# Performance work log

Hardware: AMD Instinct MI355X
Metric: run time of the kernel (lower is better)

Reference implementation:

```python
import jax, jax.numpy as jnp
import numpy as np

B_, H_, W_, DM = 32, 64, 64, 256
D_INNER, D_STATE, NHEADS, HEADDIM = 512, 64, 8, 64
D_IN_PROJ = D_INNER + 2 * D_STATE + NHEADS  # 648


def setup_inputs() -> dict:
    key = jax.random.key(0)
    ks = jax.random.split(key, 4)
    x = jax.random.normal(ks[0], (B_, H_, W_, DM), dtype=jnp.float32)
    W_in = jax.random.normal(ks[1], (DM, D_IN_PROJ), dtype=jnp.float32) * 0.05
    dt_bias = jax.random.normal(ks[2], (NHEADS,), dtype=jnp.float32)
    A_log = jax.random.uniform(ks[3], (NHEADS,), dtype=jnp.float32)  # A in [1, e)
    D_param = jnp.ones((NHEADS,), dtype=jnp.float32)
    ln_gamma = jnp.ones((D_INNER,), dtype=jnp.float32)
    ln_beta = jnp.zeros((D_INNER,), dtype=jnp.float32)
    W_out = jax.random.normal(jax.random.fold_in(key, 7), (D_INNER, DM), dtype=jnp.float32) * 0.05
    return {"x": x, "W_in": W_in, "dt_bias": dt_bias, "A_log": A_log,
            "D_param": D_param, "ln_gamma": ln_gamma, "ln_beta": ln_beta, "W_out": W_out}


def reference(x, W_in, dt_bias, A_log, D_param, ln_gamma, ln_beta, W_out):
    B, H, W, Dm = x.shape
    L = H * W
    u = x.reshape(B, L, Dm)
    A = -jnp.exp(A_log)  # (nheads,), negative
    xbcdt = u @ W_in  # (B, L, 648)
    x_ssm = xbcdt[..., :D_INNER]                          # (B, L, d_inner)
    B_ssm = xbcdt[..., D_INNER:D_INNER + D_STATE]         # (B, L, d_state) ~ K
    C_ssm = xbcdt[..., D_INNER + D_STATE:D_INNER + 2 * D_STATE]  # (B, L, d_state) ~ Q
    dt = jax.nn.softplus(xbcdt[..., D_INNER + 2 * D_STATE:] + dt_bias)  # (B, L, nheads)
    V = x_ssm.reshape(B, L, NHEADS, HEADDIM)  # (B, L, h, p)
    # dA gating: dt * A per head (defaults: no exp/softmax/norm variants)
    dA = dt * A  # (B, L, h)
    V_scaled = V * dA[..., None]  # (B, L, h, p)
    # linear-attention dual: KV = K^T @ V_scaled, then Q @ KV
    KV = jnp.einsum('bls,blhp->bhsp', B_ssm, V_scaled)  # (B, h, d_state, p)
    y = jnp.einsum('bls,bhsp->blhp', C_ssm, KV)         # (B, L, h, p)
    # D skip (per-head)
    y = y + V * D_param[None, None, :, None]
    y = y.reshape(B, L, D_INNER)
    # LayerNorm
    mu = jnp.mean(y, axis=-1, keepdims=True)
    var = jnp.var(y, axis=-1, keepdims=True)
    y = (y - mu) / jnp.sqrt(var + 1e-5) * ln_gamma + ln_beta
    out = y @ W_out
    return out.reshape(B, H, W, Dm)
```

## Files before the change

kernel.cpp:

```cpp
#include <hip/hip_runtime.h>
#include <hip/hip_bf16.h>
#include <math.h>

constexpr int B_N   = 32;
constexpr int L_N   = 4096;
constexpr int DM    = 256;
constexpr int DIN   = 512;
constexpr int DS    = 64;
constexpr int NH    = 8;
constexpr int HD    = 64;
constexpr int M_N   = B_N * L_N;
constexpr int XBW   = 640;
constexpr int YST   = 536;
constexpr int AST   = 268;

typedef unsigned short u16;
typedef short s16x4 __attribute__((ext_vector_type(4)));
typedef short s16x8 __attribute__((ext_vector_type(8)));
typedef float f32x4 __attribute__((ext_vector_type(4)));
typedef unsigned short u16x8 __attribute__((ext_vector_type(8)));
typedef unsigned short u16x4 __attribute__((ext_vector_type(4)));

__device__ __forceinline__ float softplusf(float z) {
  return (z > 20.f) ? z : log1pf(expf(z));
}
__device__ __forceinline__ u16 f2bf(float f) {
  unsigned u = __float_as_uint(f);
  u += 0x7FFFu + ((u >> 16) & 1u);
  return (u16)(u >> 16);
}
__device__ __forceinline__ float bf2f(u16 u) {
  return __uint_as_float(((unsigned)u) << 16);
}
__device__ __forceinline__ s16x8 ld_frag2(const short* p) {
  s16x4 lo = *(const s16x4*)p;
  s16x4 hi = *(const s16x4*)(p + 4);
  s16x8 r;
  r[0]=lo[0]; r[1]=lo[1]; r[2]=lo[2]; r[3]=lo[3];
  r[4]=hi[0]; r[5]=hi[1]; r[6]=hi[2]; r[7]=hi[3];
  return r;
}

#define GLDS(gsrc, ldst)                                                       \
  __builtin_amdgcn_global_load_lds(                                            \
      (const __attribute__((address_space(1))) void*)(gsrc),                   \
      (__attribute__((address_space(3))) void*)(ldst), 16, 0, 0)

constexpr long CW1 = 768L * 256;
constexpr long CW2 = CW1 + 256L * 512;
__global__ __launch_bounds__(256) void k_cvt(
    const float* __restrict__ Wi, const float* __restrict__ Wo,
    u16* __restrict__ WinT, u16* __restrict__ WoT) {
  for (long i = (long)blockIdx.x * 256 + threadIdx.x; i < CW2;
       i += (long)gridDim.x * 256) {
    if (i < CW1) {
      int n = (int)(i >> 8); int k = (int)(i & 255);
      WinT[i] = (n < 648) ? f2bf(Wi[(size_t)k * 648 + n]) : (u16)0;
    } else {
      long t = i - CW1; int n = (int)(t >> 9); int k = (int)(t & 511);
      WoT[t] = f2bf(Wo[(size_t)k * 256 + n]);
    }
  }
}

__global__ __launch_bounds__(256) void k_inproj(
    const float* __restrict__ x, const u16* __restrict__ WinT,
    const float* __restrict__ dt_bias, const float* __restrict__ A_log,
    u16* __restrict__ xbcdt, float* __restrict__ dAv) {
  __shared__ __align__(16) short sA[128 * AST];
  __shared__ __align__(16) short sB[128 * 32];
  const int tid = threadIdx.x;
  const int wave = tid >> 6, lane = tid & 63;
  const int m0 = blockIdx.x * 128;
  const int wr = wave >> 1, wc = wave & 1;
  const int fr = lane & 15, fq = lane >> 4;

#pragma unroll
  for (int q = 0; q < 32; ++q) {
    int idx = tid + q * 256;
    int row = idx >> 6, c4 = idx & 63;
    float4 v = *(const float4*)(x + (size_t)(m0 + row) * DM + c4 * 4);
    u16x4 o = {f2bf(v.x), f2bf(v.y), f2bf(v.z), f2bf(v.w)};
    *(u16x4*)&sA[row * AST + c4 * 4] = o;
  }
  __syncthreads();

  int rowB[2], kcB[2], ldsOffB[2];
#pragma unroll
  for (int q = 0; q < 2; ++q) {
    int G = wave * 128 + q * 64 + lane;
    rowB[q] = G >> 2; kcB[q] = G & 3;
    ldsOffB[q] = G * 8;
  }

  for (int nt = 0; nt < 6; ++nt) {
    const int n0 = nt * 128;
    f32x4 acc[4][4] = {};
    for (int k0 = 0; k0 < DM; k0 += 32) {
      if (nt || k0) __syncthreads();
#pragma unroll
      for (int q = 0; q < 2; ++q)
        GLDS(WinT + (size_t)(n0 + rowB[q]) * DM + kcB[q] * 8 + k0, sB + ldsOffB[q]);
      __syncthreads();
      const int kb = fq * 8;
      s16x8 af[4], bf[4];
#pragma unroll
      for (int i = 0; i < 4; ++i)
        af[i] = ld_frag2(&sA[(wr * 64 + i * 16 + fr) * AST + k0 + kb]);
#pragma unroll
      for (int j = 0; j < 4; ++j)
        bf[j] = *(const s16x8*)&sB[(wc * 64 + j * 16 + fr) * 32 + kb];
#pragma unroll
      for (int i = 0; i < 4; ++i)
#pragma unroll
        for (int j = 0; j < 4; ++j)
          acc[i][j] = __builtin_amdgcn_mfma_f32_16x16x32_bf16(af[i], bf[j], acc[i][j], 0, 0, 0);
    }
    const int row_base = m0 + wr * 64 + fq * 4;
    if (n0 < 640) {
      const int col_base = n0 + wc * 64;
#pragma unroll
      for (int i = 0; i < 4; ++i)
#pragma unroll
        for (int r = 0; r < 4; ++r) {
          int row = row_base + i * 16 + r;
#pragma unroll
          for (int j = 0; j < 4; ++j)
            xbcdt[(size_t)row * XBW + col_base + j * 16 + fr] = f2bf(acc[i][j][r]);
        }
    } else if (wc == 0 && fr < 8) {
      const float nAe = -expf(A_log[fr]);
      const float db = dt_bias[fr];
#pragma unroll
      for (int i = 0; i < 4; ++i)
#pragma unroll
        for (int r = 0; r < 4; ++r) {
          int row = row_base + i * 16 + r;
          dAv[(size_t)row * NH + fr] = softplusf(acc[i][0][r] + db) * nAe;
        }
    }
  }
}

__global__ __launch_bounds__(256) void k_bt(
    const u16* __restrict__ xbcdt, u16* __restrict__ Bt) {
  __shared__ u16 sT[64][72];
  const int m0 = blockIdx.x * 64;
  const int b  = m0 >> 12;
  const int l0 = m0 & (L_N - 1);
  const int tid = threadIdx.x;
#pragma unroll
  for (int q = 0; q < 2; ++q) {
    int r = (tid >> 3) + q * 32, c8 = (tid & 7) * 8;
    u16x8 v = *(const u16x8*)&xbcdt[(size_t)(m0 + r) * XBW + DIN + c8];
#pragma unroll
    for (int jj = 0; jj < 8; ++jj) sT[r][c8 + jj] = v[jj];
  }
  __syncthreads();
#pragma unroll
  for (int q = 0; q < 2; ++q) {
    int s = (tid >> 3) + q * 32, lc8 = (tid & 7) * 8;
    u16x8 o;
#pragma unroll
    for (int jj = 0; jj < 8; ++jj) o[jj] = sT[lc8 + jj][s];
    *(u16x8*)&Bt[((size_t)(b * 64 + s)) * L_N + l0 + lc8] = o;
  }
}

__global__ __launch_bounds__(256) void k_kv(
    const u16* __restrict__ xbcdt, const u16* __restrict__ Bt,
    const float* __restrict__ dAv, float* __restrict__ KVp) {
  const int bh = blockIdx.y;
  const int b = bh >> 3, h = bh & 7;
  const int l0 = blockIdx.x * (L_N / 4);
  const int tid = threadIdx.x;
  const int wave = tid >> 6, lane = tid & 63;
  const int wr = wave >> 1, wc = wave & 1;
  const int fr = lane & 15, fq = lane >> 4;
  __shared__ short sBt[64 * 36];
  __shared__ short sVt[64 * 36];
  f32x4 acc[2][2] = {};
  const int ts = tid >> 2, tlc = tid & 3;
  const int tl = tid >> 3, tpg = tid & 7;

  for (int ks = 0; ks < L_N / 4; ks += 32) {
    u16x8 vb = *(const u16x8*)&Bt[((size_t)(b * 64 + ts)) * L_N + l0 + ks + tlc * 8];
    const int gl = b * L_N + l0 + ks + tl;
    u16x8 vv = *(const u16x8*)&xbcdt[(size_t)gl * XBW + h * HD + tpg * 8];
    const float da = dAv[(size_t)gl * NH + h];
    __syncthreads();
    *(s16x4*)&sBt[ts * 36 + tlc * 8]     = *(s16x4*)&vb;
    *(s16x4*)&sBt[ts * 36 + tlc * 8 + 4] = *((s16x4*)&vb + 1);
#pragma unroll
    for (int jj = 0; jj < 8; ++jj)
      sVt[(tpg * 8 + jj) * 36 + tl] = (short)f2bf(bf2f(vv[jj]) * da);
    __syncthreads();
    s16x8 af[2], bf[2];
#pragma unroll
    for (int i = 0; i < 2; ++i)
      af[i] = ld_frag2(&sBt[(wr * 32 + i * 16 + fr) * 36 + fq * 8]);
#pragma unroll
    for (int j = 0; j < 2; ++j)
      bf[j] = ld_frag2(&sVt[(wc * 32 + j * 16 + fr) * 36 + fq * 8]);
#pragma unroll
    for (int i = 0; i < 2; ++i)
#pragma unroll
      for (int j = 0; j < 2; ++j)
        acc[i][j] = __builtin_amdgcn_mfma_f32_16x16x32_bf16(af[i], bf[j], acc[i][j], 0, 0, 0);
  }
  float* dst = KVp + ((size_t)(blockIdx.x * 256 + bh)) * 4096;
#pragma unroll
  for (int i = 0; i < 2; ++i)
#pragma unroll
    for (int j = 0; j < 2; ++j) {
      int p = wc * 32 + j * 16 + fr;
      int s0 = wr * 32 + i * 16 + fq * 4;
      float4 v;
      v.x = acc[i][j][0]; v.y = acc[i][j][1];
      v.z = acc[i][j][2]; v.w = acc[i][j][3];
      *(float4*)&dst[p * 64 + s0] = v;
    }
}

__global__ __launch_bounds__(256) void k_kvsum(
    const float* __restrict__ KVp, u16* __restrict__ KVt) {
  const int bh = blockIdx.x;
  const int tid = threadIdx.x;
  const float* src = KVp + (size_t)bh * 4096;
#pragma unroll
  for (int q = 0; q < 4; ++q) {
    int i4 = (tid + q * 256) * 4;
    float4 v0 = *(const float4*)(src + i4);
    float4 v1 = *(const float4*)(src + 1048576 + i4);
    float4 v2 = *(const float4*)(src + 2097152 + i4);
    float4 v3 = *(const float4*)(src + 3145728 + i4);
    u16x4 o = {f2bf(v0.x + v1.x + v2.x + v3.x),
               f2bf(v0.y + v1.y + v2.y + v3.y),
               f2bf(v0.z + v1.z + v2.z + v3.z),
               f2bf(v0.w + v1.w + v2.w + v3.w)};
    *(u16x4*)&KVt[(size_t)bh * 4096 + i4] = o;
  }
}

__global__ __launch_bounds__(256) void k_fused(
    const u16* __restrict__ xb, const u16* __restrict__ KVt,
    const float* __restrict__ Dp, const float* __restrict__ g,
    const float* __restrict__ bt, const u16* __restrict__ WoT,
    float* __restrict__ out) {
  __shared__ __align__(16) short sC[64 * 76];
  __shared__ __align__(16) short sY[64 * YST];
  const int tid = threadIdx.x;
  const int wave = tid >> 6, lane = tid & 63;
  const int fr = lane & 15, fq = lane >> 4;
  const int m0 = blockIdx.x * 64;
  const int b = m0 >> 12;

#pragma unroll
  for (int q = 0; q < 2; ++q) {
    int idx = tid + q * 256;
    int row = idx >> 3, c8 = (idx & 7) * 8;
    u16x8 v = *(const u16x8*)&xb[(size_t)(m0 + row) * XBW + DIN + DS + c8];
    *(u16x8*)&sC[row * 76 + c8] = v;
  }

  {
    s16x8 ktf[2][4];
    const u16* kt0 = KVt + (size_t)(b * NH + wave) * 4096;
#pragma unroll
    for (int kk = 0; kk < 2; ++kk)
#pragma unroll
      for (int i = 0; i < 4; ++i)
        ktf[kk][i] = *(const s16x8*)&kt0[(i * 16 + fr) * 64 + kk * 32 + fq * 8];
    __syncthreads();

    s16x8 cf[2][4];
#pragma unroll
    for (int kk = 0; kk < 2; ++kk)
#pragma unroll
      for (int j = 0; j < 4; ++j)
        cf[kk][j] = *(const s16x8*)&sC[(j * 16 + fr) * 76 + kk * 32 + fq * 8];

#pragma unroll
    for (int hh = 0; hh < 2; ++hh) {
      const int h = wave + hh * 4;
      f32x4 acc[4][4] = {};
#pragma unroll
      for (int kk = 0; kk < 2; ++kk)
#pragma unroll
        for (int i = 0; i < 4; ++i)
#pragma unroll
          for (int j = 0; j < 4; ++j)
            acc[i][j] = __builtin_amdgcn_mfma_f32_16x16x32_bf16(ktf[kk][i], cf[kk][j], acc[i][j], 0, 0, 0);
      if (hh == 0) {
        const u16* kt1 = KVt + (size_t)(b * NH + wave + 4) * 4096;
#pragma unroll
        for (int kk = 0; kk < 2; ++kk)
#pragma unroll
          for (int i = 0; i < 4; ++i)
            ktf[kk][i] = *(const s16x8*)&kt1[(i * 16 + fr) * 64 + kk * 32 + fq * 8];
      }
#pragma unroll
      for (int i = 0; i < 4; ++i)
#pragma unroll
        for (int j = 0; j < 4; ++j) {
          u16x4 o = {f2bf(acc[i][j][0]), f2bf(acc[i][j][1]),
                     f2bf(acc[i][j][2]), f2bf(acc[i][j][3])};
          *(u16x4*)&sY[(j * 16 + fr) * YST + h * 64 + i * 16 + fq * 4] = o;
        }
    }
  }
  __syncthreads();

  {
    const int row = tid >> 2, seg4 = tid & 3;
    const u16* vrow = xb + (size_t)(m0 + row) * XBW;
    float s = 0.f, q = 0.f;
#pragma unroll
    for (int c = 0; c < 16; ++c) {
      int k0 = seg4 * 8 + c * 32;
      const float ds = Dp[c >> 1];
      u16x8 v = *(const u16x8*)&sY[row * YST + k0];
      u16x8 w = *(const u16x8*)(vrow + k0);
      u16x8 o;
#pragma unroll
      for (int jj = 0; jj < 8; ++jj) {
        float f = bf2f(v[jj]) + ds * bf2f(w[jj]);
        s += f; q += f * f;
        o[jj] = f2bf(f);
      }
      *(u16x8*)&sY[row * YST + k0] = o;
    }
    s += __shfl_xor(s, 1); q += __shfl_xor(q, 1);
    s += __shfl_xor(s, 2); q += __shfl_xor(q, 2);
    const float mu = s / DIN;
    const float rstd = rsqrtf(q / DIN - mu * mu + 1e-5f);
#pragma unroll
    for (int c = 0; c < 16; ++c) {
      int k0 = seg4 * 8 + c * 32;
      u16x8 v = *(const u16x8*)&sY[row * YST + k0];
      float4 g0 = *(const float4*)(g + k0);
      float4 g1 = *(const float4*)(g + k0 + 4);
      float4 b0 = *(const float4*)(bt + k0);
      float4 b1 = *(const float4*)(bt + k0 + 4);
      u16x8 o;
      o[0] = f2bf((bf2f(v[0]) - mu) * rstd * g0.x + b0.x);
      o[1] = f2bf((bf2f(v[1]) - mu) * rstd * g0.y + b0.y);
      o[2] = f2bf((bf2f(v[2]) - mu) * rstd * g0.z + b0.z);
      o[3] = f2bf((bf2f(v[3]) - mu) * rstd * g0.w + b0.w);
      o[4] = f2bf((bf2f(v[4]) - mu) * rstd * g1.x + b1.x);
      o[5] = f2bf((bf2f(v[5]) - mu) * rstd * g1.y + b1.y);
      o[6] = f2bf((bf2f(v[6]) - mu) * rstd * g1.z + b1.z);
      o[7] = f2bf((bf2f(v[7]) - mu) * rstd * g1.w + b1.w);
      *(u16x8*)&sY[row * YST + k0] = o;
    }
  }
  __syncthreads();

  {
    f32x4 acc2[4][4] = {};
#pragma unroll
    for (int kk = 0; kk < 16; ++kk) {
      s16x8 af2[4], bf2[4];
#pragma unroll
      for (int i = 0; i < 4; ++i)
        af2[i] = *(const s16x8*)&sY[(i * 16 + fr) * YST + kk * 32 + fq * 8];
#pragma unroll
      for (int j = 0; j < 4; ++j)
        bf2[j] = *(const s16x8*)&WoT[(size_t)(wave * 64 + j * 16 + fr) * DIN + kk * 32 + fq * 8];
#pragma unroll
      for (int i = 0; i < 4; ++i)
#pragma unroll
        for (int j = 0; j < 4; ++j)
          acc2[i][j] = __builtin_amdgcn_mfma_f32_16x16x32_bf16(af2[i], bf2[j], acc2[i][j], 0, 0, 0);
    }
#pragma unroll
    for (int i = 0; i < 4; ++i)
#pragma unroll
      for (int r = 0; r < 4; ++r) {
        int row = m0 + i * 16 + fq * 4 + r;
#pragma unroll
        for (int j = 0; j < 4; ++j)
          out[(size_t)row * DM + wave * 64 + j * 16 + fr] = acc2[i][j][r];
      }
  }
}

extern "C" void kernel_launch(void* const* d_in, const int* in_sizes, int n_in,
                              void* d_out, int out_size, void* d_ws, size_t ws_size,
                              hipStream_t stream) {
  const float* x       = (const float*)d_in[0];
  const float* W_in    = (const float*)d_in[1];
  const float* dt_bias = (const float*)d_in[2];
  const float* A_log   = (const float*)d_in[3];
  const float* D_param = (const float*)d_in[4];
  const float* gamma   = (const float*)d_in[5];
  const float* beta    = (const float*)d_in[6];
  const float* W_out   = (const float*)d_in[7];
  float* out = (float*)d_out;

  u16* ws    = (u16*)d_ws;
  u16* WinT  = ws;
  u16* WoT   = WinT + 768L * 256;
  u16* xbcdt = WoT + 256L * 512;
  u16* Bt    = xbcdt + (size_t)M_N * XBW;
  float* dAv = (float*)(Bt + (size_t)B_N * 64 * L_N);
  float* KVp = dAv + (size_t)M_N * NH;
  u16* KVt   = (u16*)(KVp + 4L * 256 * 4096);

  k_cvt    <<<256, 256, 0, stream>>>(W_in, W_out, WinT, WoT);
  k_inproj <<<M_N / 128, 256, 0, stream>>>(x, WinT, dt_bias, A_log, xbcdt, dAv);
  k_bt     <<<M_N / 64, 256, 0, stream>>>(xbcdt, Bt);
  k_kv     <<<dim3(4, B_N * NH), 256, 0, stream>>>(xbcdt, Bt, dAv, KVp);
  k_kvsum  <<<B_N * NH, 256, 0, stream>>>(KVp, KVt);
  k_fused  <<<M_N / 64, 256, 0, stream>>>(xbcdt, KVt, D_param, gamma, beta, WoT, out);
}
```

Before: 283.9 us.

## Fuse B transpose into in-projection epilogue and raise MFMA wave priority

The in-projection GEMM epilogue now writes the B_ssm columns straight into the transposed Bt layout, so the separate k_bt transpose kernel and its reread of xbcdt are gone. C columns are still written to xbcdt. s_setprio is also wrapped around the MFMA loops in the fused output kernel so those waves get higher issue priority. The transposed stores are 8-byte chunks strided by L, which are less coalesced than the old row-major writes.

```diff
diff --git a/kernel.cpp b/kernel.cpp
--- a/kernel.cpp
+++ b/kernel.cpp
@@ -66,7 +66,7 @@
 __global__ __launch_bounds__(256) void k_inproj(
     const float* __restrict__ x, const u16* __restrict__ WinT,
     const float* __restrict__ dt_bias, const float* __restrict__ A_log,
-    u16* __restrict__ xbcdt, float* __restrict__ dAv) {
+    u16* __restrict__ xbcdt, u16* __restrict__ Bt, float* __restrict__ dAv) {
   __shared__ __align__(16) short sA[128 * AST];
   __shared__ __align__(16) short sB[128 * 32];
   const int tid = threadIdx.x;
@@ -117,7 +117,7 @@
           acc[i][j] = __builtin_amdgcn_mfma_f32_16x16x32_bf16(af[i], bf[j], acc[i][j], 0, 0, 0);
     }
     const int row_base = m0 + wr * 64 + fq * 4;
-    if (n0 < 640) {
+    if (n0 < 512 || (nt == 4 && wc == 1)) {
       const int col_base = n0 + wc * 64;
 #pragma unroll
       for (int i = 0; i < 4; ++i)
@@ -128,7 +128,19 @@
           for (int j = 0; j < 4; ++j)
             xbcdt[(size_t)row * XBW + col_base + j * 16 + fr] = f2bf(acc[i][j][r]);
         }
-    } else if (wc == 0 && fr < 8) {
+    } else if (nt == 4) {
+      const int b = row_base >> 12;
+      const int l_base = (row_base & (L_N - 1));
+#pragma unroll
+      for (int i = 0; i < 4; ++i)
+#pragma unroll
+        for (int j = 0; j < 4; ++j) {
+          int s = j * 16 + fr;
+          u16x4 pk = {f2bf(acc[i][j][0]), f2bf(acc[i][j][1]),
+                      f2bf(acc[i][j][2]), f2bf(acc[i][j][3])};
+          *(u16x4*)&Bt[((size_t)(b * 64 + s)) * L_N + l_base + i * 16] = pk;
+        }
+    } else if (nt == 5 && wc == 0 && fr < 8) {
       const float nAe = -expf(A_log[fr]);
       const float db = dt_bias[fr];
 #pragma unroll
@@ -139,31 +151,6 @@
           dAv[(size_t)row * NH + fr] = softplusf(acc[i][0][r] + db) * nAe;
         }
     }
-  }
-}
-
-__global__ __launch_bounds__(256) void k_bt(
-    const u16* __restrict__ xbcdt, u16* __restrict__ Bt) {
-  __shared__ u16 sT[64][72];
-  const int m0 = blockIdx.x * 64;
-  const int b  = m0 >> 12;
-  const int l0 = m0 & (L_N - 1);
-  const int tid = threadIdx.x;
-#pragma unroll
-  for (int q = 0; q < 2; ++q) {
-    int r = (tid >> 3) + q * 32, c8 = (tid & 7) * 8;
-    u16x8 v = *(const u16x8*)&xbcdt[(size_t)(m0 + r) * XBW + DIN + c8];
-#pragma unroll
-    for (int jj = 0; jj < 8; ++jj) sT[r][c8 + jj] = v[jj];
-  }
-  __syncthreads();
-#pragma unroll
-  for (int q = 0; q < 2; ++q) {
-    int s = (tid >> 3) + q * 32, lc8 = (tid & 7) * 8;
-    u16x8 o;
-#pragma unroll
-    for (int jj = 0; jj < 8; ++jj) o[jj] = sT[lc8 + jj][s];
-    *(u16x8*)&Bt[((size_t)(b * 64 + s)) * L_N + l0 + lc8] = o;
   }
 }
 
@@ -284,6 +271,7 @@
     for (int hh = 0; hh < 2; ++hh) {
       const int h = wave + hh * 4;
       f32x4 acc[4][4] = {};
+      __builtin_amdgcn_s_setprio(1);
 #pragma unroll
       for (int kk = 0; kk < 2; ++kk)
 #pragma unroll
@@ -291,6 +279,7 @@
 #pragma unroll
           for (int j = 0; j < 4; ++j)
             acc[i][j] = __builtin_amdgcn_mfma_f32_16x16x32_bf16(ktf[kk][i], cf[kk][j], acc[i][j], 0, 0, 0);
+      __builtin_amdgcn_s_setprio(0);
       if (hh == 0) {
         const u16* kt1 = KVt + (size_t)(b * NH + wave + 4) * 4096;
 #pragma unroll
@@ -367,11 +356,13 @@
 #pragma unroll
       for (int j = 0; j < 4; ++j)
         bf2[j] = *(const s16x8*)&WoT[(size_t)(wave * 64 + j * 16 + fr) * DIN + kk * 32 + fq * 8];
+      __builtin_amdgcn_s_setprio(1);
 #pragma unroll
       for (int i = 0; i < 4; ++i)
 #pragma unroll
         for (int j = 0; j < 4; ++j)
           acc2[i][j] = __builtin_amdgcn_mfma_f32_16x16x32_bf16(af2[i], bf2[j], acc2[i][j], 0, 0, 0);
+      __builtin_amdgcn_s_setprio(0);
     }
 #pragma unroll
     for (int i = 0; i < 4; ++i)
@@ -408,8 +399,7 @@
   u16* KVt   = (u16*)(KVp + 4L * 256 * 4096);
 
   k_cvt    <<<256, 256, 0, stream>>>(W_in, W_out, WinT, WoT);
-  k_inproj <<<M_N / 128, 256, 0, stream>>>(x, WinT, dt_bias, A_log, xbcdt, dAv);
-  k_bt     <<<M_N / 64, 256, 0, stream>>>(xbcdt, Bt);
+  k_inproj <<<M_N / 128, 256, 0, stream>>>(x, WinT, dt_bias, A_log, xbcdt, Bt, dAv);
   k_kv     <<<dim3(4, B_N * NH), 256, 0, stream>>>(xbcdt, Bt, dAv, KVp);
   k_kvsum  <<<B_N * NH, 256, 0, stream>>>(KVp, KVt);
   k_fused  <<<M_N / 64, 256, 0, stream>>>(xbcdt, KVt, D_param, gamma, beta, WoT, out);
```

Result: no change. 280.7 us (-1.1%).
